# Kernel optimization log

Measured on AMD Instinct MI355X. Metric: run time of the kernel, lower is better.

## Reference

```python
import jax, jax.numpy as jnp
import numpy as np

H = 1024   # hidden_size
S = 32768  # seq_len


def setup_inputs() -> dict:
    key = jax.random.key(0)
    k1, k2, k3, k4 = jax.random.split(key, 4)
    scale = 1.0 / np.sqrt(H)
    return {
        "hidden": jax.random.normal(k1, (H,), dtype=jnp.float32),
        "encoder_outputs": jax.random.normal(k2, (S, H), dtype=jnp.float32),
        "W": jax.random.normal(k3, (H, H), dtype=jnp.float32) * scale,
        "b": jax.random.normal(k4, (H,), dtype=jnp.float32) * scale,
    }


def reference(hidden, encoder_outputs, W, b):
    # method == 'general': energy_i = W @ enc_i + b ; score_i = hidden . energy_i
    # Vectorized: scores = (enc @ W^T + b) @ hidden  -> [S]
    energies = jnp.einsum("sh,dh->sd", encoder_outputs, W) + b  # [S, H]
    scores = energies @ hidden                                   # [S]
    attn = jax.nn.softmax(scores)                                 # softmax over seq_len
    return attn[None, None, :]                                    # [1, 1, S]
```

## Files before the change

kernel.cpp:

```cpp
#include <hip/hip_runtime.h>
#include <math.h>

#define H 1024
#define S 32768
#define NPART 16
#define RPW 8
#define NB2 1024

#define WS_PART   0
#define WS_PM     16384
#define WS_PS     17408
#define WS_SCORES 18432

__global__ __launch_bounds__(256) void matvec_partial(const float* __restrict__ W,
                                                      const float* __restrict__ hidden,
                                                      float* __restrict__ ws) {
    float* part = ws + WS_PART;
    const int t  = threadIdx.x;
    const int l  = t & 63;
    const int dg = t >> 6;
    const int h  = blockIdx.x * 64 + l;
    const int d0 = blockIdx.y * 64 + dg * 16;

    float acc = 0.f;
#pragma unroll
    for (int i = 0; i < 16; ++i)
        acc += W[(size_t)(d0 + i) * H + h] * hidden[d0 + i];

    __shared__ float red[4][64];
    red[dg][l] = acc;
    __syncthreads();
    if (t < 64)
        part[blockIdx.y * H + blockIdx.x * 64 + l] =
            red[0][l] + red[1][l] + red[2][l] + red[3][l];
}

__device__ __forceinline__ float4 add4(float4 a, float4 b) {
    return make_float4(a.x + b.x, a.y + b.y, a.z + b.z, a.w + b.w);
}

__device__ __forceinline__ float dot16(const float4 e0, const float4 e1,
                                       const float4 e2, const float4 e3,
                                       const float4 vf[4]) {
    float s0 = e0.x * vf[0].x + e0.y * vf[0].y + e0.z * vf[0].z + e0.w * vf[0].w;
    float s1 = e1.x * vf[1].x + e1.y * vf[1].y + e1.z * vf[1].z + e1.w * vf[1].w;
    float s2 = e2.x * vf[2].x + e2.y * vf[2].y + e2.z * vf[2].z + e2.w * vf[2].w;
    float s3 = e3.x * vf[3].x + e3.y * vf[3].y + e3.z * vf[3].z + e3.w * vf[3].w;
    return (s0 + s1) + (s2 + s3);
}

__global__ __launch_bounds__(256) void scores_partial(const float* __restrict__ enc,
                                                      float* __restrict__ ws) {
    float* scores = ws + WS_SCORES;
    float* pm     = ws + WS_PM;
    float* ps     = ws + WS_PS;
    const float* part = ws + WS_PART;

    const int tid  = threadIdx.x;
    const int lane = tid & 63;
    const int wv   = tid >> 6;
    const int blk  = blockIdx.x;
    const int gw   = blk * 4 + wv;
    const size_t row0 = (size_t)gw * RPW;

    const float4* e4 = (const float4*)(enc + row0 * H);
    float4 p00 = e4[lane],       p01 = e4[lane + 64],
           p02 = e4[lane + 128], p03 = e4[lane + 192];
    float4 p10 = e4[256 + lane],       p11 = e4[256 + lane + 64],
           p12 = e4[256 + lane + 128], p13 = e4[256 + lane + 192];

    __shared__ float vsh[H];
    {
        const float4* p4 = (const float4*)part;
        float4 t[NPART];
#pragma unroll
        for (int p = 0; p < NPART; ++p) t[p] = p4[p * (H / 4) + tid];
#pragma unroll
        for (int p = 0; p < 8; ++p) t[p] = add4(t[p], t[p + 8]);
#pragma unroll
        for (int p = 0; p < 4; ++p) t[p] = add4(t[p], t[p + 4]);
        ((float4*)vsh)[tid] = add4(add4(t[0], t[2]), add4(t[1], t[3]));
    }
    __syncthreads();

    const float4* v4 = (const float4*)vsh;
    float4 vf[4];
#pragma unroll
    for (int k = 0; k < 4; ++k) vf[k] = v4[lane + 64 * k];

    float a[RPW];
    a[0] = dot16(p00, p01, p02, p03, vf);
    a[1] = dot16(p10, p11, p12, p13, vf);
#pragma unroll
    for (int it = 2; it < RPW; ++it) {
        const float4* r = e4 + it * 256;
        a[it] = dot16(r[lane], r[lane + 64], r[lane + 128], r[lane + 192], vf);
    }

#pragma unroll
    for (int it = 0; it < RPW; ++it) {
#pragma unroll
        for (int off = 32; off > 0; off >>= 1)
            a[it] += __shfl_xor(a[it], off, 64);
    }
    if (lane == 0) {
        *(float4*)(scores + row0)     = make_float4(a[0], a[1], a[2], a[3]);
        *(float4*)(scores + row0 + 4) = make_float4(a[4], a[5], a[6], a[7]);
    }

    float m01 = fmaxf(a[0], a[1]), m23 = fmaxf(a[2], a[3]);
    float m45 = fmaxf(a[4], a[5]), m67 = fmaxf(a[6], a[7]);
    const float mw = fmaxf(fmaxf(m01, m23), fmaxf(m45, m67));
    float sw = 0.f;
#pragma unroll
    for (int it = 0; it < RPW; ++it) sw += __expf(a[it] - mw);

    __shared__ float sm[4], ss[4];
    if (lane == 0) { sm[wv] = mw; ss[wv] = sw; }
    __syncthreads();
    if (tid == 0) {
        float m = sm[0], s = ss[0];
#pragma unroll
        for (int i = 1; i < 4; ++i) {
            const float nm = fmaxf(m, sm[i]);
            s = s * __expf(m - nm) + ss[i] * __expf(sm[i] - nm);
            m = nm;
        }
        pm[blk] = m; ps[blk] = s;
    }
}

__global__ __launch_bounds__(256) void finalize(const float* __restrict__ ws,
                                                float* __restrict__ out) {
    const float* scores = ws + WS_SCORES;
    const float* pm     = ws + WS_PM;
    const float* ps     = ws + WS_PS;

    const int tid  = threadIdx.x;
    const int lane = tid & 63;
    const int wv   = tid >> 6;

    float m = -INFINITY, s = 0.f;
#pragma unroll
    for (int i = 0; i < NB2 / 256; ++i) {
        const int idx = tid + i * 256;
        const float om = pm[idx], os = ps[idx];
        const float nm = fmaxf(m, om);
        s = s * __expf(m - nm) + os * __expf(om - nm);
        m = nm;
    }
#pragma unroll
    for (int off = 32; off > 0; off >>= 1) {
        const float om = __shfl_xor(m, off, 64);
        const float os = __shfl_xor(s, off, 64);
        const float nm = fmaxf(m, om);
        s = s * __expf(m - nm) + os * __expf(om - nm);
        m = nm;
    }
    __shared__ float sm[4], ss[4];
    if (lane == 0) { sm[wv] = m; ss[wv] = s; }
    __syncthreads();
    float M = sm[0], Ssum = ss[0];
#pragma unroll
    for (int i = 1; i < 4; ++i) {
        const float nm = fmaxf(M, sm[i]);
        Ssum = Ssum * __expf(M - nm) + ss[i] * __expf(sm[i] - nm);
        M = nm;
    }
    const float rs = 1.0f / Ssum;

    const int i = blockIdx.x * 256 + tid;
    out[i] = __expf(scores[i] - M) * rs;
}

extern "C" void kernel_launch(void* const* d_in, const int* in_sizes, int n_in,
                              void* d_out, int out_size, void* d_ws, size_t ws_size,
                              hipStream_t stream) {
    const float* hidden = (const float*)d_in[0];
    const float* enc    = (const float*)d_in[1];
    const float* W      = (const float*)d_in[2];
    float* out = (float*)d_out;
    float* ws  = (float*)d_ws;

    matvec_partial<<<dim3(16, 16), 256, 0, stream>>>(W, hidden, ws);
    scores_partial<<<NB2, 256, 0, stream>>>(enc, ws);
    finalize<<<S / 256, 256, 0, stream>>>(ws, out);
}
```

Before: 201.3 us.

## Fuse softmax finalize into scores kernel via atomic ticket last-block reduction

Removes the separate finalize launch. Each scores block takes a ticket from an atomic counter that matvec_partial resets. The last NWORK blocks spin until every block has arrived, then compute the global max and sum and normalize 4096 outputs each. This saves one kernel launch and its gap, but only 8 blocks do the normalization, and they spin-wait, which relies on all blocks eventually being scheduled.

After: 250.1 us. 1.24x slower.

```diff
diff --git a/kernel.cpp b/kernel.cpp
--- a/kernel.cpp
+++ b/kernel.cpp
@@ -6,16 +6,21 @@
 #define NPART 16
 #define RPW 8
 #define NB2 1024
+#define NWORK 8
 
 #define WS_PART   0
 #define WS_PM     16384
 #define WS_PS     17408
 #define WS_SCORES 18432
+#define WS_CTR    51200
 
 __global__ __launch_bounds__(256) void matvec_partial(const float* __restrict__ W,
                                                       const float* __restrict__ hidden,
                                                       float* __restrict__ ws) {
     float* part = ws + WS_PART;
+    if (blockIdx.x == 0 && blockIdx.y == 0 && threadIdx.x == 0)
+        *(int*)(ws + WS_CTR) = 0;
+
     const int t  = threadIdx.x;
     const int l  = t & 63;
     const int dg = t >> 6;
@@ -50,11 +55,13 @@
 }
 
 __global__ __launch_bounds__(256) void scores_partial(const float* __restrict__ enc,
-                                                      float* __restrict__ ws) {
+                                                      float* __restrict__ ws,
+                                                      float* __restrict__ out) {
     float* scores = ws + WS_SCORES;
     float* pm     = ws + WS_PM;
     float* ps     = ws + WS_PS;
     const float* part = ws + WS_PART;
+    int* ctr = (int*)(ws + WS_CTR);
 
     const int tid  = threadIdx.x;
     const int lane = tid & 63;
@@ -128,17 +135,28 @@
         }
         pm[blk] = m; ps[blk] = s;
     }
-}
-
-__global__ __launch_bounds__(256) void finalize(const float* __restrict__ ws,
-                                                float* __restrict__ out) {
-    const float* scores = ws + WS_SCORES;
-    const float* pm     = ws + WS_PM;
-    const float* ps     = ws + WS_PS;
-
-    const int tid  = threadIdx.x;
-    const int lane = tid & 63;
-    const int wv   = tid >> 6;
+
+    __shared__ int ticket_sh;
+    __syncthreads();
+    if (tid == 0)
+        ticket_sh = __hip_atomic_fetch_add(ctr, 1, __ATOMIC_RELEASE,
+                                           __HIP_MEMORY_SCOPE_AGENT);
+    __syncthreads();
+    const int ticket = ticket_sh;
+    if (ticket < NB2 - NWORK) return;
+
+    const int w = ticket - (NB2 - NWORK);
+
+    if (tid == 0) {
+        int guard = 0;
+        while (__hip_atomic_load(ctr, __ATOMIC_RELAXED,
+                                 __HIP_MEMORY_SCOPE_AGENT) < NB2) {
+            __builtin_amdgcn_s_sleep(1);
+            if (++guard > 100000000) break;
+        }
+    }
+    __syncthreads();
+    __threadfence();
 
     float m = -INFINITY, s = 0.f;
 #pragma unroll
@@ -157,7 +175,7 @@
         s = s * __expf(m - nm) + os * __expf(om - nm);
         m = nm;
     }
-    __shared__ float sm[4], ss[4];
+    __syncthreads();
     if (lane == 0) { sm[wv] = m; ss[wv] = s; }
     __syncthreads();
     float M = sm[0], Ssum = ss[0];
@@ -169,8 +187,16 @@
     }
     const float rs = 1.0f / Ssum;
 
-    const int i = blockIdx.x * 256 + tid;
-    out[i] = __expf(scores[i] - M) * rs;
+    const float4* sc4 = (const float4*)scores + w * 1024;
+    float4* out4      = (float4*)out + w * 1024;
+#pragma unroll
+    for (int j = 0; j < 4; ++j) {
+        const float4 sv = sc4[j * 256 + tid];
+        out4[j * 256 + tid] = make_float4(__expf(sv.x - M) * rs,
+                                          __expf(sv.y - M) * rs,
+                                          __expf(sv.z - M) * rs,
+                                          __expf(sv.w - M) * rs);
+    }
 }
 
 extern "C" void kernel_launch(void* const* d_in, const int* in_sizes, int n_in,
@@ -183,6 +209,5 @@
     float* ws  = (float*)d_ws;
 
     matvec_partial<<<dim3(16, 16), 256, 0, stream>>>(W, hidden, ws);
-    scores_partial<<<NB2, 256, 0, stream>>>(enc, ws);
-    finalize<<<S / 256, 256, 0, stream>>>(ws, out);
-}
+    scores_partial<<<NB2, 256, 0, stream>>>(enc, ws, out);
+}
```
